# Kernel tuning notes

Hardware: AMD Instinct MI355X
Metric: run time of the kernel (lower is better)

## Reference

```python
import jax, jax.numpy as jnp
import numpy as np

HEADS = 8
DIM_HEAD = 64
GROUPS = 32  # min(dim//4, 32) with dim=256
EPS = 1e-5

def setup_inputs() -> dict:
    key = jax.random.key(0)
    ks = jax.random.split(key, 5)
    C, H, W = 256, 256, 256
    hidden = HEADS * DIM_HEAD  # 512
    x = jax.random.normal(ks[0], (C, H, W), dtype=jnp.float32)
    gn_w = jnp.ones((C,), dtype=jnp.float32)
    gn_b = jnp.zeros((C,), dtype=jnp.float32)
    qkv_w = jax.random.normal(ks[1], (3 * hidden, C), dtype=jnp.float32) * (1.0 / np.sqrt(C))
    qkv_b = jax.random.normal(ks[2], (3 * hidden,), dtype=jnp.float32) * 0.02
    out_w = jax.random.normal(ks[3], (C, hidden), dtype=jnp.float32) * (1.0 / np.sqrt(hidden))
    out_b = jax.random.normal(ks[4], (C,), dtype=jnp.float32) * 0.02
    return {"x": x, "gn_w": gn_w, "gn_b": gn_b, "qkv_w": qkv_w,
            "qkv_b": qkv_b, "out_w": out_w, "out_b": out_b}

def reference(x, gn_w, gn_b, qkv_w, qkv_b, out_w, out_b):
    C, H, W = x.shape
    n = H * W
    # GroupNorm over (channels-in-group, h, w)
    xg = x.reshape(GROUPS, C // GROUPS, H, W)
    mean = xg.mean(axis=(1, 2, 3), keepdims=True)
    var = xg.var(axis=(1, 2, 3), keepdims=True)
    xn = ((xg - mean) * jax.lax.rsqrt(var + EPS)).reshape(C, H, W)
    xn = xn * gn_w[:, None, None] + gn_b[:, None, None]
    # 1x1 conv QKV projection
    qkv = jnp.einsum('oc,chw->ohw', qkv_w, xn) + qkv_b[:, None, None]
    # split as '(qkv heads c) h w -> qkv heads c (h w)'
    q, k, v = qkv.reshape(3, HEADS, DIM_HEAD, n)
    k = jax.nn.softmax(k, axis=-1)  # softmax over spatial axis
    context = jnp.einsum('hdn,hen->hde', k, v)   # [heads, d, d] small
    out = jnp.einsum('hde,hdn->hen', context, q)  # [heads, d, n]
    out = out.reshape(HEADS * DIM_HEAD, H, W)
    # 1x1 conv output projection
    return jnp.einsum('oc,chw->ohw', out_w, out) + out_b[:, None, None]
```

## Files before the change

### kernel.cpp

```cpp
#include <hip/hip_runtime.h>
#include <stdint.h>

typedef __attribute__((ext_vector_type(8))) short bf16x8;
typedef __attribute__((ext_vector_type(4))) float f32x4;
typedef __attribute__((ext_vector_type(4))) unsigned int u32x4;

#define NSP 65536

#define WS_XN     0ULL
#define WS_WFRAG  33554432ULL
#define WS_WEFRAG 34078720ULL
#define WS_PART   34209792ULL
#define WS_AB     34211840ULL
#define WS_CTX    34215936ULL
#define WS_W2     34347008ULL
#define WS_WEFF   35395584ULL
#define WS_BEFF   35657728ULL


__device__ __forceinline__ unsigned short f2bf(float f) {
  union { float f; uint32_t u; } v; v.f = f;
  uint32_t r = v.u + 0x7FFFu + ((v.u >> 16) & 1u);
  return (unsigned short)(r >> 16);
}
__device__ __forceinline__ float bf2f(unsigned short b) {
  union { uint32_t u; float f; } v; v.u = ((uint32_t)b) << 16;
  return v.f;
}

__global__ void k_stats(const float* __restrict__ x, float* __restrict__ part) {
  __shared__ float ss[256], sq[256];
  const int t = threadIdx.x, b = blockIdx.x;
  const f32x4* p = (const f32x4*)(x + (size_t)b * 65536);
  float s = 0.f, qq = 0.f;
  for (int k = 0; k < 64; ++k) {
    f32x4 v = __builtin_nontemporal_load(p + t + 256 * k);
    s  += v[0] + v[1] + v[2] + v[3];
    qq += v[0] * v[0] + v[1] * v[1] + v[2] * v[2] + v[3] * v[3];
  }
  ss[t] = s; sq[t] = qq;
  __syncthreads();
  for (int st = 128; st > 0; st >>= 1) {
    if (t < st) { ss[t] += ss[t + st]; sq[t] += sq[t + st]; }
    __syncthreads();
  }
  if (t == 0) { part[2 * b] = ss[0]; part[2 * b + 1] = sq[0]; }
}

__global__ void k_coef(const float* __restrict__ part, const float* __restrict__ gn_w,
                       const float* __restrict__ gn_b, float* __restrict__ ab) {
  const int c = threadIdx.x;
  const int g = c >> 3;
  float s = 0.f, q = 0.f;
  for (int j = 0; j < 8; ++j) { s += part[(g * 8 + j) * 2]; q += part[(g * 8 + j) * 2 + 1]; }
  const float inv = 1.0f / 524288.0f;
  const float mean = s * inv;
  const float var = q * inv - mean * mean;
  const float rstd = rsqrtf(var + 1e-5f);
  const float a = gn_w[c] * rstd;
  ab[c] = a;
  ab[256 + c] = gn_b[c] - mean * a;
}

__global__ void k_xn(const float* __restrict__ x, const float* __restrict__ ab,
                     unsigned short* __restrict__ xn, unsigned short* __restrict__ xnf) {
  __shared__ float tile[64][66];
  const int t = threadIdx.x;
  const int nb = blockIdx.x, cb = blockIdx.y;
  {
    const int cl = t >> 2, nc = t & 3;
    const int c = cb * 64 + cl;
    const float a = ab[c], b = ab[256 + c];
    const f32x4* src = (const f32x4*)(x + (size_t)c * NSP + nb * 64 + nc * 16);
#pragma unroll
    for (int j = 0; j < 4; ++j) {
      f32x4 v = __builtin_nontemporal_load(src + j);
      v = v * a + b;
      *(f32x4*)&tile[cl][nc * 16 + j * 4] = v;
    }
  }
  __syncthreads();
#pragma unroll
  for (int pass = 0; pass < 2; ++pass) {
    const int nl = pass * 32 + (t >> 3);
    const int ch = t & 7;
    const int u = ch ^ (nl & 7);
    union { unsigned short s[8]; u32x4 v; } pkv;
#pragma unroll
    for (int e = 0; e < 8; ++e) pkv.s[e] = f2bf(tile[u * 8 + e][nl]);
    *(u32x4*)(xn + (size_t)(nb * 64 + nl) * 256 + cb * 64 + ch * 8) = pkv.v;
  }
  {
    const int l = t & 63, w0 = t >> 6;
    u32x4* xnf4 = (u32x4*)xnf;
#pragma unroll
    for (int u2 = 0; u2 < 2; ++u2) {
      const int fp = w0 + u2 * 4;
      const int fl = fp >> 1, ksl = fp & 1;
      union { unsigned short s[8]; u32x4 v; } pk2;
#pragma unroll
      for (int e = 0; e < 8; ++e)
        pk2.s[e] = f2bf(tile[ksl * 32 + (l >> 4) * 8 + e][fl * 16 + (l & 15)]);
      xnf4[((size_t)(nb * 4 + fl) * 8 + cb * 2 + ksl) * 64 + l] = pk2.v;
    }
  }
}

__global__ void k_wfrag(const float* __restrict__ qkv_w, unsigned short* __restrict__ wf) {
  const int blk = blockIdx.x;
  const int l = threadIdx.x;
  const int row = 512 + (blk & 63) * 16 + (l & 15);
  const int c0 = (blk >> 6) * 32 + (l >> 4) * 8;
  const float* src = qkv_w + (size_t)row * 256 + c0;
  union { unsigned short s[8]; u32x4 v; } u;
#pragma unroll
  for (int j = 0; j < 8; ++j) u.s[j] = f2bf(src[j]);
  *(u32x4*)(wf + ((size_t)blk * 64 + l) * 8) = u.v;
}

__launch_bounds__(512, 1)
__global__ void k_kvctx(const unsigned short* __restrict__ xnf,
                        const unsigned short* __restrict__ wfrag,
                        const float* __restrict__ qkv_b,
                        float* __restrict__ sump, float* __restrict__ ctxp) {
  __shared__ __align__(16) char lds[133120];
  const int t = threadIdx.x;
  const int w = t >> 6, l = t & 63;
  const int q = l & 15;
  const int h = blockIdx.x >> 5;
  const int chunk = blockIdx.x & 31;

  {
    const u32x4* wsrc = (const u32x4*)wfrag;
    u32x4* wdst = (u32x4*)lds;
#pragma unroll
    for (int r = 0; r < 8; ++r) {
      const int e = r * 512 + t;
      const int entry = e >> 6, l2 = e & 63;
      const int ph = entry >> 5, ks = (entry >> 2) & 7, jj = entry & 3;
      wdst[e] = wsrc[((size_t)(ks * 64 + ph * 32 + h * 4 + jj)) * 64 + l2];
    }
  }

  const f32x4 fz = {0.f, 0.f, 0.f, 0.f};
  f32x4 ctxa[4][4];
#pragma unroll
  for (int a = 0; a < 4; ++a)
#pragma unroll
    for (int b = 0; b < 4; ++b) ctxa[a][b] = fz;
  float srow[4] = {0.f, 0.f, 0.f, 0.f};
  float bk[4], bv[4];
#pragma unroll
  for (int jj = 0; jj < 4; ++jj) {
    bk[jj] = qkv_b[512 + h * 64 + jj * 16 + q];
    bv[jj] = qkv_b[1024 + h * 64 + jj * 16 + q];
  }

  const u32x4* xsrc = (const u32x4*)xnf + (size_t)chunk * 65536;
  u32x4* xa4 = (u32x4*)(lds + 65536);

  for (int tt = 0; tt < 16; ++tt) {
    __syncthreads();
#pragma unroll
    for (int r = 0; r < 8; ++r)
      xa4[r * 512 + t] = xsrc[(size_t)tt * 4096 + r * 512 + t];
    __syncthreads();

    f32x4 ak[4] = {fz, fz, fz, fz};
#pragma unroll
    for (int ks = 0; ks < 8; ++ks) {
      const bf16x8 xa = *(const bf16x8*)(lds + 65536 + ((w * 8 + ks) * 64 + l) * 16);
#pragma unroll
      for (int jj = 0; jj < 4; ++jj) {
        const bf16x8 bwk = *(const bf16x8*)(lds + ((ks * 4 + jj) * 64 + l) * 16);
        ak[jj] = __builtin_amdgcn_mfma_f32_16x16x32_bf16(xa, bwk, ak[jj], 0, 0, 0);
      }
    }
    bf16x8 pk[4];
#pragma unroll
    for (int jj = 0; jj < 4; ++jj) {
      float s = 0.f;
      bf16x8 p = {0, 0, 0, 0, 0, 0, 0, 0};
#pragma unroll
      for (int r = 0; r < 4; ++r) {
        const unsigned short u0 = f2bf(__expf(ak[jj][r] + bk[jj]));
        p[r] = (short)u0;
        s += bf2f(u0);
      }
      pk[jj] = p;
      srow[jj] += s;
    }

    f32x4 av[4] = {fz, fz, fz, fz};
#pragma unroll
    for (int ks = 0; ks < 8; ++ks) {
      const bf16x8 xa = *(const bf16x8*)(lds + 65536 + ((w * 8 + ks) * 64 + l) * 16);
#pragma unroll
      for (int jj = 0; jj < 4; ++jj) {
        const bf16x8 bwv = *(const bf16x8*)(lds + (((8 + ks) * 4 + jj) * 64 + l) * 16);
        av[jj] = __builtin_amdgcn_mfma_f32_16x16x32_bf16(xa, bwv, av[jj], 0, 0, 0);
      }
    }
    bf16x8 pv[4];
#pragma unroll
    for (int jj = 0; jj < 4; ++jj) {
      bf16x8 p = {0, 0, 0, 0, 0, 0, 0, 0};
#pragma unroll
      for (int r = 0; r < 4; ++r)
        p[r] = (short)f2bf(av[jj][r] + bv[jj]);
      pv[jj] = p;
    }

#pragma unroll
    for (int ja = 0; ja < 4; ++ja)
#pragma unroll
      for (int jb = 0; jb < 4; ++jb)
        ctxa[ja][jb] = __builtin_amdgcn_mfma_f32_16x16x32_bf16(pk[ja], pv[jb], ctxa[ja][jb], 0, 0, 0);
  }

  __syncthreads();
  {
    float* dw = (float*)lds + w * 4096 + l * 4;
#pragma unroll
    for (int ja = 0; ja < 4; ++ja)
#pragma unroll
      for (int jb = 0; jb < 4; ++jb)
        *(f32x4*)(dw + (ja * 4 + jb) * 256) = ctxa[ja][jb];
  }
  {
    float* srl = (float*)(lds + 131072);
#pragma unroll
    for (int jj = 0; jj < 4; ++jj) {
      float s = srow[jj];
      s += __shfl_xor(s, 16, 64);
      s += __shfl_xor(s, 32, 64);
      if (l < 16) srl[w * 64 + jj * 16 + q] = s;
    }
  }
  __syncthreads();
  {
    const float* dump = (const float*)lds;
#pragma unroll
    for (int j = 0; j < 2; ++j) {
      const int m4 = j * 512 + t;
      f32x4 s = fz;
#pragma unroll
      for (int w8 = 0; w8 < 8; ++w8)
        s += *(const f32x4*)(dump + w8 * 4096 + m4 * 4);
      *(f32x4*)(ctxp + ((size_t)(h * 32 + chunk) * 1024 + m4) * 4) = s;
    }
    if (t < 64) {
      const float* srl = (const float*)(lds + 131072);
      float s = 0.f;
#pragma unroll
      for (int w8 = 0; w8 < 8; ++w8) s += srl[w8 * 64 + t];
      sump[(size_t)(h * 64 + t) * 32 + chunk] = s;
    }
  }
}

__global__ void k_ctxred(const float* __restrict__ ctxp, const float* __restrict__ sump,
                         float* __restrict__ ctx, float* __restrict__ sexp) {
  const int t = threadIdx.x;
  if (blockIdx.x < 64) {
    const int m4 = blockIdx.x * 128 + t;
    const int h = m4 >> 10, p4 = m4 & 1023;
    f32x4 s = {0.f, 0.f, 0.f, 0.f};
#pragma unroll 8
    for (int c = 0; c < 32; ++c)
      s += *(const f32x4*)(ctxp + (((size_t)h * 32 + c) * 1024 + p4) * 4);
    const int jajb = p4 >> 6, ll = p4 & 63;
    const int ja = jajb >> 2, jb = jajb & 3;
    const int gg = ll >> 4, qq = ll & 15;
    float* cw = ctx + ((size_t)h * 64 + ja * 16 + gg * 4) * 64 + jb * 16 + qq;
    cw[0] = s[0]; cw[64] = s[1]; cw[128] = s[2]; cw[192] = s[3];
  } else {
    const int r = (blockIdx.x - 64) * 128 + t;
    float s = 0.f;
#pragma unroll 8
    for (int c = 0; c < 32; ++c) s += sump[(size_t)r * 32 + c];
    sexp[r] = s;
  }
}

__global__ void k_w2(const float* __restrict__ out_w, const float* __restrict__ ctx,
                     const float* __restrict__ sexp, float* __restrict__ w2) {
  const int r = blockIdx.x;
  const int h = r >> 6, d = r & 63;
  __shared__ float row[64];
  __shared__ float sinv;
  const int t = threadIdx.x;
  if (t < 64) row[t] = ctx[((size_t)h * 64 + d) * 64 + t];
  if (t == 0) sinv = 1.0f / sexp[r];
  __syncthreads();
  float a = 0.f;
  const float* wp = out_w + (size_t)t * 512 + h * 64;
#pragma unroll 8
  for (int e = 0; e < 64; ++e) a += wp[e] * row[e];
  w2[(size_t)t * 512 + r] = a * sinv;
}

__global__ void k_weff(const float* __restrict__ w2, const float* __restrict__ qkv_w,
                       float* __restrict__ weff) {
  const int o = blockIdx.x;
  const int c = threadIdx.x;
  __shared__ float row[512];
  row[c] = w2[(size_t)o * 512 + c];
  row[256 + c] = w2[(size_t)o * 512 + 256 + c];
  __syncthreads();
  float a = 0.f;
#pragma unroll 8
  for (int r = 0; r < 512; ++r) a += row[r] * qkv_w[(size_t)r * 256 + c];
  weff[o * 256 + c] = a;
}

__global__ void k_wefrag(const float* __restrict__ weff, unsigned short* __restrict__ wf) {
  const int blk = blockIdx.x;
  const int l = threadIdx.x;
  const int row = (blk & 15) * 16 + (l & 15);
  const int c0 = (blk >> 4) * 32 + (l >> 4) * 8;
  const float* src = weff + (size_t)row * 256 + c0;
  union { unsigned short s[8]; u32x4 v; } u;
#pragma unroll
  for (int j = 0; j < 8; ++j) u.s[j] = f2bf(src[j]);
  *(u32x4*)(wf + ((size_t)blk * 64 + l) * 8) = u.v;
}

__global__ void k_beff(const float* __restrict__ w2, const float* __restrict__ qkv_b,
                       const float* __restrict__ out_b, float* __restrict__ beff) {
  const int o = threadIdx.x;
  float a = out_b[o];
#pragma unroll 8
  for (int r = 0; r < 512; ++r) a += w2[(size_t)o * 512 + r] * qkv_b[r];
  beff[o] = a;
}

__launch_bounds__(256, 2)
__global__ void k_final(const unsigned short* __restrict__ xn,
                        const unsigned short* __restrict__ wef,
                        const float* __restrict__ beff,
                        float* __restrict__ out) {
  __shared__ unsigned short xlds[32768];
  const int t = threadIdx.x;
  const int w = t >> 6, l = t & 63;
  const int q = l & 15, g = l >> 4;
  const int si = w >> 1, sj = w & 1;
  const size_t n0 = (size_t)blockIdx.x * 128;
  {
    const u32x4* gs = (const u32x4*)(xn + n0 * 256);
    u32x4* ld = (u32x4*)xlds;
#pragma unroll
    for (int k2 = 0; k2 < 16; ++k2) {
      u32x4 v = __builtin_nontemporal_load(gs + t + 256 * k2);
      ld[t + 256 * k2] = v;
    }
  }
  __syncthreads();
  const f32x4 fz = {0.f, 0.f, 0.f, 0.f};
  f32x4 acc[4][8];
#pragma unroll
  for (int i = 0; i < 4; ++i)
#pragma unroll
    for (int j = 0; j < 8; ++j) acc[i][j] = fz;
#pragma unroll
  for (int ks = 0; ks < 8; ++ks) {
    bf16x8 xa[4];
#pragma unroll
    for (int i = 0; i < 4; ++i) {
      const int nl = si * 64 + i * 16 + q;
      const int boff = nl * 512 + ((ks * 64 + g * 16) ^ ((nl & 7) << 4));
      xa[i] = *(const bf16x8*)((const char*)xlds + boff);
    }
#pragma unroll
    for (int jj = 0; jj < 8; ++jj) {
      const bf16x8 bw = *(const bf16x8*)(wef + (((size_t)(ks * 16 + sj * 8 + jj)) * 64 + l) * 8);
#pragma unroll
      for (int i = 0; i < 4; ++i)
        acc[i][jj] = __builtin_amdgcn_mfma_f32_16x16x32_bf16(xa[i], bw, acc[i][jj], 0, 0, 0);
    }
  }
  __syncthreads();
  float* trf = (float*)xlds;
#pragma unroll
  for (int k4 = 0; k4 < 4; ++k4) {
    if ((k4 >> 1) == sj) {
#pragma unroll
      for (int jj2 = 0; jj2 < 4; ++jj2) {
        const int jj = (k4 & 1) * 4 + jj2;
        const float be = beff[sj * 128 + jj * 16 + q];
#pragma unroll
        for (int i = 0; i < 4; ++i)
#pragma unroll
          for (int r = 0; r < 4; ++r)
            trf[(jj2 * 16 + q) * 129 + si * 64 + i * 16 + g * 4 + r] = acc[i][jj][r] + be;
      }
    }
    __syncthreads();
#pragma unroll
    for (int j = 0; j < 32; ++j) {
      const int mm = j * 256 + t;
      const int ol = mm >> 7, cc = mm & 127;
      out[(size_t)(k4 * 64 + ol) * NSP + n0 + cc] = trf[ol * 129 + cc];
    }
    __syncthreads();
  }
}

extern "C" void kernel_launch(void* const* d_in, const int* in_sizes, int n_in,
                              void* d_out, int out_size, void* d_ws, size_t ws_size,
                              hipStream_t stream) {
  const float* x     = (const float*)d_in[0];
  const float* gn_w  = (const float*)d_in[1];
  const float* gn_b  = (const float*)d_in[2];
  const float* qkv_w = (const float*)d_in[3];
  const float* qkv_b = (const float*)d_in[4];
  const float* out_w = (const float*)d_in[5];
  const float* out_b = (const float*)d_in[6];
  char* ws = (char*)d_ws;
  unsigned short* xn  = (unsigned short*)(ws + WS_XN);
  unsigned short* wf  = (unsigned short*)(ws + WS_WFRAG);
  unsigned short* wef = (unsigned short*)(ws + WS_WEFRAG);
  float* part   = (float*)(ws + WS_PART);
  float* ab     = (float*)(ws + WS_AB);
  float* ctx    = (float*)(ws + WS_CTX);
  float* w2     = (float*)(ws + WS_W2);
  float* weff   = (float*)(ws + WS_WEFF);
  float* beff   = (float*)(ws + WS_BEFF);
  float* out    = (float*)d_out;
  unsigned short* xnf = (unsigned short*)d_out;
  float* ctxp = (float*)((char*)d_out + 33554432ULL);
  float* sump = (float*)((char*)d_out + 37748736ULL);

  k_wfrag<<<512, 64, 0, stream>>>(qkv_w, wf);
  k_stats<<<256, 256, 0, stream>>>(x, part);
  k_coef<<<1, 256, 0, stream>>>(part, gn_w, gn_b, ab);
  k_xn<<<dim3(1024, 4), 256, 0, stream>>>(x, ab, xn, xnf);
  k_kvctx<<<256, 512, 0, stream>>>(xnf, wf, qkv_b, sump, ctxp);
  k_ctxred<<<68, 128, 0, stream>>>(ctxp, sump, ctx, part);
  k_w2<<<512, 256, 0, stream>>>(out_w, ctx, part, w2);
  k_weff<<<256, 256, 0, stream>>>(w2, qkv_w, weff);
  k_wefrag<<<128, 64, 0, stream>>>(weff, wef);
  k_beff<<<1, 256, 0, stream>>>(w2, qkv_b, out_b, beff);
  k_final<<<512, 256, 0, stream>>>(xn, wef, beff, out);
}
```

Measured before the change: 194.1 us.

## Drop duplicate normalized-x buffer and reuse fragment layout in final GEMM

The normalize kernel now writes only the MFMA-fragment-layout bf16 copy of the normalized input, moved into the workspace, instead of also writing a row-major copy. The final projection kernel reads that fragment layout straight into LDS, and the KV-context kernel handles two row groups per step, one staged in LDS and one read directly from global, so the K/V weight fragments are reused across twice as many rows. The bias-effective kernel is folded into the weff kernel as a block reduction. This removes one 32 MB write and a launch, but adds uncoalesced-risk direct global fragment loads inside the MFMA loop.

```diff
diff --git a/kernel.cpp b/kernel.cpp
--- a/kernel.cpp
+++ b/kernel.cpp
@@ -63,7 +63,7 @@
 }
 
 __global__ void k_xn(const float* __restrict__ x, const float* __restrict__ ab,
-                     unsigned short* __restrict__ xn, unsigned short* __restrict__ xnf) {
+                     unsigned short* __restrict__ xnf) {
   __shared__ float tile[64][66];
   const int t = threadIdx.x;
   const int nb = blockIdx.x, cb = blockIdx.y;
@@ -80,16 +80,6 @@
     }
   }
   __syncthreads();
-#pragma unroll
-  for (int pass = 0; pass < 2; ++pass) {
-    const int nl = pass * 32 + (t >> 3);
-    const int ch = t & 7;
-    const int u = ch ^ (nl & 7);
-    union { unsigned short s[8]; u32x4 v; } pkv;
-#pragma unroll
-    for (int e = 0; e < 8; ++e) pkv.s[e] = f2bf(tile[u * 8 + e][nl]);
-    *(u32x4*)(xn + (size_t)(nb * 64 + nl) * 256 + cb * 64 + ch * 8) = pkv.v;
-  }
   {
     const int l = t & 63, w0 = t >> 6;
     u32x4* xnf4 = (u32x4*)xnf;
@@ -156,58 +146,67 @@
     bv[jj] = qkv_b[1024 + h * 64 + jj * 16 + q];
   }
 
-  const u32x4* xsrc = (const u32x4*)xnf + (size_t)chunk * 65536;
+  const u32x4* xnf4 = (const u32x4*)xnf;
   u32x4* xa4 = (u32x4*)(lds + 65536);
 
-  for (int tt = 0; tt < 16; ++tt) {
+  for (int st = 0; st < 8; ++st) {
+    const size_t rg0 = (size_t)chunk * 128 + st * 16;
     __syncthreads();
 #pragma unroll
     for (int r = 0; r < 8; ++r)
-      xa4[r * 512 + t] = xsrc[(size_t)tt * 4096 + r * 512 + t];
-    __syncthreads();
-
-    f32x4 ak[4] = {fz, fz, fz, fz};
+      xa4[r * 512 + t] = xnf4[rg0 * 512 + r * 512 + t];
+    __syncthreads();
+    const u32x4* gB = xnf4 + (rg0 + 8 + w) * 512 + l;
+
+    f32x4 ak[2][4] = {{fz, fz, fz, fz}, {fz, fz, fz, fz}};
 #pragma unroll
     for (int ks = 0; ks < 8; ++ks) {
-      const bf16x8 xa = *(const bf16x8*)(lds + 65536 + ((w * 8 + ks) * 64 + l) * 16);
+      const bf16x8 xaA = *(const bf16x8*)(lds + 65536 + ((w * 8 + ks) * 64 + l) * 16);
+      const bf16x8 xaB = *(const bf16x8*)(gB + ks * 64);
 #pragma unroll
       for (int jj = 0; jj < 4; ++jj) {
         const bf16x8 bwk = *(const bf16x8*)(lds + ((ks * 4 + jj) * 64 + l) * 16);
-        ak[jj] = __builtin_amdgcn_mfma_f32_16x16x32_bf16(xa, bwk, ak[jj], 0, 0, 0);
+        ak[0][jj] = __builtin_amdgcn_mfma_f32_16x16x32_bf16(xaA, bwk, ak[0][jj], 0, 0, 0);
+        ak[1][jj] = __builtin_amdgcn_mfma_f32_16x16x32_bf16(xaB, bwk, ak[1][jj], 0, 0, 0);
       }
     }
     bf16x8 pk[4];
 #pragma unroll
     for (int jj = 0; jj < 4; ++jj) {
       float s = 0.f;
-      bf16x8 p = {0, 0, 0, 0, 0, 0, 0, 0};
+      bf16x8 p;
 #pragma unroll
       for (int r = 0; r < 4; ++r) {
-        const unsigned short u0 = f2bf(__expf(ak[jj][r] + bk[jj]));
-        p[r] = (short)u0;
-        s += bf2f(u0);
+        const unsigned short u0 = f2bf(__expf(ak[0][jj][r] + bk[jj]));
+        const unsigned short u1 = f2bf(__expf(ak[1][jj][r] + bk[jj]));
+        p[r] = (short)u0; p[r + 4] = (short)u1;
+        s += bf2f(u0) + bf2f(u1);
       }
       pk[jj] = p;
       srow[jj] += s;
     }
 
-    f32x4 av[4] = {fz, fz, fz, fz};
+    f32x4 av[2][4] = {{fz, fz, fz, fz}, {fz, fz, fz, fz}};
 #pragma unroll
     for (int ks = 0; ks < 8; ++ks) {
-      const bf16x8 xa = *(const bf16x8*)(lds + 65536 + ((w * 8 + ks) * 64 + l) * 16);
+      const bf16x8 xaA = *(const bf16x8*)(lds + 65536 + ((w * 8 + ks) * 64 + l) * 16);
+      const bf16x8 xaB = *(const bf16x8*)(gB + ks * 64);
 #pragma unroll
       for (int jj = 0; jj < 4; ++jj) {
         const bf16x8 bwv = *(const bf16x8*)(lds + (((8 + ks) * 4 + jj) * 64 + l) * 16);
-        av[jj] = __builtin_amdgcn_mfma_f32_16x16x32_bf16(xa, bwv, av[jj], 0, 0, 0);
+        av[0][jj] = __builtin_amdgcn_mfma_f32_16x16x32_bf16(xaA, bwv, av[0][jj], 0, 0, 0);
+        av[1][jj] = __builtin_amdgcn_mfma_f32_16x16x32_bf16(xaB, bwv, av[1][jj], 0, 0, 0);
       }
     }
     bf16x8 pv[4];
 #pragma unroll
     for (int jj = 0; jj < 4; ++jj) {
-      bf16x8 p = {0, 0, 0, 0, 0, 0, 0, 0};
-#pragma unroll
-      for (int r = 0; r < 4; ++r)
-        p[r] = (short)f2bf(av[jj][r] + bv[jj]);
+      bf16x8 p;
+#pragma unroll
+      for (int r = 0; r < 4; ++r) {
+        p[r]     = (short)f2bf(av[0][jj][r] + bv[jj]);
+        p[r + 4] = (short)f2bf(av[1][jj][r] + bv[jj]);
+      }
       pv[jj] = p;
     }
 
@@ -240,10 +239,11 @@
   __syncthreads();
   {
     const float* dump = (const float*)lds;
+    const f32x4 fz2 = {0.f, 0.f, 0.f, 0.f};
 #pragma unroll
     for (int j = 0; j < 2; ++j) {
       const int m4 = j * 512 + t;
-      f32x4 s = fz;
+      f32x4 s = fz2;
 #pragma unroll
       for (int w8 = 0; w8 < 8; ++w8)
         s += *(const f32x4*)(dump + w8 * 4096 + m4 * 4);
@@ -301,10 +301,12 @@
 }
 
 __global__ void k_weff(const float* __restrict__ w2, const float* __restrict__ qkv_w,
-                       float* __restrict__ weff) {
+                       const float* __restrict__ qkv_b, const float* __restrict__ out_b,
+                       float* __restrict__ weff, float* __restrict__ beff) {
   const int o = blockIdx.x;
   const int c = threadIdx.x;
   __shared__ float row[512];
+  __shared__ float red[256];
   row[c] = w2[(size_t)o * 512 + c];
   row[256 + c] = w2[(size_t)o * 512 + 256 + c];
   __syncthreads();
@@ -312,6 +314,13 @@
 #pragma unroll 8
   for (int r = 0; r < 512; ++r) a += row[r] * qkv_w[(size_t)r * 256 + c];
   weff[o * 256 + c] = a;
+  red[c] = row[c] * qkv_b[c] + row[256 + c] * qkv_b[256 + c];
+  __syncthreads();
+  for (int st = 128; st > 0; st >>= 1) {
+    if (c < st) red[c] += red[c + st];
+    __syncthreads();
+  }
+  if (c == 0) beff[o] = out_b[o] + red[0];
 }
 
 __global__ void k_wefrag(const float* __restrict__ weff, unsigned short* __restrict__ wf) {
@@ -326,17 +335,8 @@
   *(u32x4*)(wf + ((size_t)blk * 64 + l) * 8) = u.v;
 }
 
-__global__ void k_beff(const float* __restrict__ w2, const float* __restrict__ qkv_b,
-                       const float* __restrict__ out_b, float* __restrict__ beff) {
-  const int o = threadIdx.x;
-  float a = out_b[o];
-#pragma unroll 8
-  for (int r = 0; r < 512; ++r) a += w2[(size_t)o * 512 + r] * qkv_b[r];
-  beff[o] = a;
-}
-
 __launch_bounds__(256, 2)
-__global__ void k_final(const unsigned short* __restrict__ xn,
+__global__ void k_final(const unsigned short* __restrict__ xnf,
                         const unsigned short* __restrict__ wef,
                         const float* __restrict__ beff,
                         float* __restrict__ out) {
@@ -347,13 +347,11 @@
   const int si = w >> 1, sj = w & 1;
   const size_t n0 = (size_t)blockIdx.x * 128;
   {
-    const u32x4* gs = (const u32x4*)(xn + n0 * 256);
+    const u32x4* gs = (const u32x4*)xnf + (size_t)blockIdx.x * 4096;
     u32x4* ld = (u32x4*)xlds;
 #pragma unroll
-    for (int k2 = 0; k2 < 16; ++k2) {
-      u32x4 v = __builtin_nontemporal_load(gs + t + 256 * k2);
-      ld[t + 256 * k2] = v;
-    }
+    for (int k2 = 0; k2 < 16; ++k2)
+      ld[t + 256 * k2] = gs[t + 256 * k2];
   }
   __syncthreads();
   const f32x4 fz = {0.f, 0.f, 0.f, 0.f};
@@ -366,11 +364,8 @@
   for (int ks = 0; ks < 8; ++ks) {
     bf16x8 xa[4];
 #pragma unroll
-    for (int i = 0; i < 4; ++i) {
-      const int nl = si * 64 + i * 16 + q;
-      const int boff = nl * 512 + ((ks * 64 + g * 16) ^ ((nl & 7) << 4));
-      xa[i] = *(const bf16x8*)((const char*)xlds + boff);
-    }
+    for (int i = 0; i < 4; ++i)
+      xa[i] = *(const bf16x8*)((const char*)xlds + (((si * 4 + i) * 8 + ks) * 64 + l) * 16);
 #pragma unroll
     for (int jj = 0; jj < 8; ++jj) {
       const bf16x8 bw = *(const bf16x8*)(wef + (((size_t)(ks * 16 + sj * 8 + jj)) * 64 + l) * 8);
@@ -417,7 +412,7 @@
   const float* out_w = (const float*)d_in[5];
   const float* out_b = (const float*)d_in[6];
   char* ws = (char*)d_ws;
-  unsigned short* xn  = (unsigned short*)(ws + WS_XN);
+  unsigned short* xnf = (unsigned short*)(ws + WS_XN);
   unsigned short* wf  = (unsigned short*)(ws + WS_WFRAG);
   unsigned short* wef = (unsigned short*)(ws + WS_WEFRAG);
   float* part   = (float*)(ws + WS_PART);
@@ -427,19 +422,17 @@
   float* weff   = (float*)(ws + WS_WEFF);
   float* beff   = (float*)(ws + WS_BEFF);
   float* out    = (float*)d_out;
-  unsigned short* xnf = (unsigned short*)d_out;
   float* ctxp = (float*)((char*)d_out + 33554432ULL);
   float* sump = (float*)((char*)d_out + 37748736ULL);
 
   k_wfrag<<<512, 64, 0, stream>>>(qkv_w, wf);
   k_stats<<<256, 256, 0, stream>>>(x, part);
   k_coef<<<1, 256, 0, stream>>>(part, gn_w, gn_b, ab);
-  k_xn<<<dim3(1024, 4), 256, 0, stream>>>(x, ab, xn, xnf);
+  k_xn<<<dim3(1024, 4), 256, 0, stream>>>(x, ab, xnf);
   k_kvctx<<<256, 512, 0, stream>>>(xnf, wf, qkv_b, sump, ctxp);
   k_ctxred<<<68, 128, 0, stream>>>(ctxp, sump, ctx, part);
   k_w2<<<512, 256, 0, stream>>>(out_w, ctx, part, w2);
-  k_weff<<<256, 256, 0, stream>>>(w2, qkv_w, weff);
+  k_weff<<<256, 256, 0, stream>>>(w2, qkv_w, qkv_b, out_b, weff, beff);
   k_wefrag<<<128, 64, 0, stream>>>(weff, wef);
-  k_beff<<<1, 256, 0, stream>>>(w2, qkv_b, out_b, beff);
-  k_final<<<512, 256, 0, stream>>>(xn, wef, beff, out);
-}
+  k_final<<<512, 256, 0, stream>>>(xnf, wef, beff, out);
+}
```

After: 172.2 us. 1.13x faster.
